# Performance work log

Measured on AMD Instinct MI355X. Metric: run time of the kernel, lower is better.

## Reference

```python
import jax, jax.numpy as jnp
from jax import lax
import numpy as np

B = 32768
H = 7
W = 7
EMB = 64
NUM_ACTIONS = 7
HIDDEN = 128
CNN_OUT = 64 * 3 * 3  # 576, from 7x7 input through the conv/pool stack


def setup_inputs() -> dict:
    key = jax.random.key(0)
    ks = jax.random.split(key, 20)
    frame = jax.random.randint(ks[0], (2, B, H, W, 3), 0, 11, dtype=jnp.int32)
    carried_col = jax.random.randint(ks[1], (2, B, 1), 0, 6, dtype=jnp.int32)
    carried_obj = jax.random.randint(ks[2], (2, B, 1), 0, 11, dtype=jnp.int32)

    def w(k, shape):
        return (jax.random.normal(k, shape, jnp.float32) * 0.05)

    return {
        "frame": frame,
        "carried_col": carried_col,
        "carried_obj": carried_obj,
        "conv1_w": w(ks[3], (16, 3, 2, 2)),  "conv1_b": jnp.zeros((16,), jnp.float32),
        "conv2_w": w(ks[4], (32, 16, 2, 2)), "conv2_b": jnp.zeros((32,), jnp.float32),
        "conv3_w": w(ks[5], (64, 32, 2, 2)), "conv3_b": jnp.zeros((64,), jnp.float32),
        "proj_w": w(ks[6], (EMB, CNN_OUT + 2)), "proj_b": jnp.zeros((EMB,), jnp.float32),
        "h1_w": w(ks[7], (HIDDEN, EMB * 2 + 4)), "h1_b": jnp.zeros((HIDDEN,), jnp.float32),
        "ln_g": jnp.ones((HIDDEN,), jnp.float32), "ln_b": jnp.zeros((HIDDEN,), jnp.float32),
        "h2_w": w(ks[8], (HIDDEN, HIDDEN)), "h2_b": jnp.zeros((HIDDEN,), jnp.float32),
        "h3_w": w(ks[9], (NUM_ACTIONS, HIDDEN)), "h3_b": jnp.zeros((NUM_ACTIONS,), jnp.float32),
    }


def _conv(x, wgt, b):
    # Conv2d(kernel=2, padding=1), NCHW
    y = lax.conv_general_dilated(x, wgt, (1, 1), [(1, 1), (1, 1)],
                                 dimension_numbers=("NCHW", "OIHW", "NCHW"))
    return y + b[None, :, None, None]


def _maxpool2(x):
    # MaxPool2d(2): window 2, stride 2, floor (VALID)
    return lax.reduce_window(x, -jnp.inf, lax.max, (1, 1, 2, 2), (1, 1, 2, 2), "VALID")


def _encode(fr, cc, co, p):
    x = fr.transpose(0, 3, 1, 2).astype(jnp.float32)  # [B,3,H,W]
    x = _maxpool2(jax.nn.relu(_conv(x, p["conv1_w"], p["conv1_b"])))  # [B,16,4,4]
    x = _maxpool2(jax.nn.relu(_conv(x, p["conv2_w"], p["conv2_b"])))  # [B,32,2,2]
    x = jax.nn.relu(_conv(x, p["conv3_w"], p["conv3_b"]))             # [B,64,3,3]
    feats = x.reshape(x.shape[0], -1)                                  # [B,576]
    carried = jnp.concatenate([cc, co], axis=-1).astype(jnp.float32)   # [B,2]
    comb = jnp.concatenate([feats, carried], axis=1)                   # [B,578]
    return jax.nn.relu(comb @ p["proj_w"].T + p["proj_b"])            # [B,64]


def _dir_pos(fr):
    # vectorized first-match of frame[...,0]==10 in row-major order
    b = fr.shape[0]
    mask = (fr[..., 0] == 10).reshape(b, -1)             # [B, H*W]
    has = jnp.any(mask, axis=-1)                         # [B]
    idx = jnp.argmax(mask, axis=-1)                      # first True (row-major)
    y = idx // W
    x = idx % W
    ch2 = fr[..., 2].reshape(b, -1)
    d_raw = jnp.take_along_axis(ch2, idx[:, None], axis=1)[:, 0] % 4
    d = jnp.where(has, d_raw, 0)                         # [B] int
    pos = jnp.stack([y.astype(jnp.float32) / (H - 1),
                     x.astype(jnp.float32) / (W - 1)], axis=-1)
    pos = jnp.where(has[:, None], pos, jnp.float32(0.5))  # [B,2]
    return d, pos


def _forward(frame, carried_col, carried_obj, p):
    curr_f, next_f = frame[0], frame[1]
    curr_emb = _encode(curr_f, carried_col[0], carried_obj[0], p)
    next_emb = _encode(next_f, carried_col[1], carried_obj[1], p)
    cd, cpos = _dir_pos(curr_f)
    nd, npos = _dir_pos(next_f)
    delta = ((nd - cd + 4) % 4).astype(jnp.float32)
    angle = delta * (2.0 * 3.14159 / 4.0)  # matches source constant
    dir_delta = jnp.stack([jnp.sin(angle), jnp.cos(angle)], axis=-1)  # [B,2]
    pos_delta = npos - cpos                                           # [B,2]
    comb = jnp.concatenate([curr_emb, next_emb, dir_delta, pos_delta], axis=-1)  # [B,132]
    h = comb @ p["h1_w"].T + p["h1_b"]
    mu = h.mean(-1, keepdims=True)
    var = ((h - mu) ** 2).mean(-1, keepdims=True)
    h = (h - mu) * lax.rsqrt(var + 1e-5) * p["ln_g"] + p["ln_b"]
    h = jax.nn.relu(h)  # dropout = identity in eval
    h = jax.nn.relu(h @ p["h2_w"].T + p["h2_b"])
    return h @ p["h3_w"].T + p["h3_b"]  # [B, num_actions]


def reference(frame, carried_col, carried_obj,
              conv1_w, conv1_b, conv2_w, conv2_b, conv3_w, conv3_b,
              proj_w, proj_b, h1_w, h1_b, ln_g, ln_b,
              h2_w, h2_b, h3_w, h3_b):
    p = dict(conv1_w=conv1_w, conv1_b=conv1_b, conv2_w=conv2_w, conv2_b=conv2_b,
             conv3_w=conv3_w, conv3_b=conv3_b, proj_w=proj_w, proj_b=proj_b,
             h1_w=h1_w, h1_b=h1_b, ln_g=ln_g, ln_b=ln_b,
             h2_w=h2_w, h2_b=h2_b, h3_w=h3_w, h3_b=h3_b)
    return _forward(frame, carried_col, carried_obj, p)
```

## Files before the change

### kernel.cpp

```cpp
#include <hip/hip_runtime.h>
#include <hip/hip_bf16.h>

#define BATCH 32768
#define NELEM 65536

typedef unsigned short u16;
typedef unsigned int u32;
typedef __attribute__((ext_vector_type(8))) short bf16x8;
typedef __attribute__((ext_vector_type(4))) float f32x4;

__device__ __forceinline__ float bf2f(u16 u) {
    union { u32 u; float f; } c; c.u = ((u32)u) << 16; return c.f;
}
__device__ __forceinline__ u16 f2bf(float f) {
    union { float f; u32 u; } c; c.f = f;
    u32 x = c.u;
    u32 r = (x + 0x7fffu + ((x >> 16) & 1u)) >> 16;
    return (u16)r;
}

__global__ __launch_bounds__(256) void k0_prep(const float* __restrict__ pw,
        const float* __restrict__ w2, const float* __restrict__ w3,
        const float* __restrict__ h2w, const float* __restrict__ h1w,
        const float* __restrict__ w1,
        u16* __restrict__ pwT, u16* __restrict__ w2r, u16* __restrict__ w3r,
        u16* __restrict__ h2hi, u16* __restrict__ h2lo,
        u16* __restrict__ h1hi, u16* __restrict__ h1lo,
        u16* __restrict__ w1hi, u16* __restrict__ w1lo) {
    int idx = blockIdx.x * 256 + threadIdx.x;
    if (idx < 38912) {
        int j = idx / 608, kk = idx - j * 608;
        float v = 0.f;
        if (kk < 576) {
            int p = kk >> 6, oc = kk & 63;
            v = pw[j * 578 + oc * 9 + p];
        } else if (kk < 578) {
            v = pw[j * 578 + kk];
        }
        pwT[idx] = f2bf(v);
    } else if (idx < 40960) {
        int i = idx - 38912;
        int oc = i >> 6, rem = i & 63, tap = rem >> 4, ic = rem & 15;
        w2r[i] = f2bf(w2[oc * 64 + ic * 4 + tap]);
    } else if (idx < 49152) {
        int i = idx - 40960;
        int oc = i >> 7, rem = i & 127, tap = rem >> 5, ic = rem & 31;
        w3r[i] = f2bf(w3[oc * 128 + ic * 4 + tap]);
    } else if (idx < 65536) {
        int i = idx - 49152;
        float v = h2w[i];
        u16 hi = f2bf(v);
        h2hi[i] = hi;
        h2lo[i] = f2bf(v - bf2f(hi));
    } else if (idx < 86016) {
        int i = idx - 65536;
        int j = i / 160, k = i - j * 160;
        float v = (k < 132) ? h1w[j * 132 + k] : 0.f;
        u16 hi = f2bf(v);
        h1hi[i] = hi;
        h1lo[i] = f2bf(v - bf2f(hi));
    } else if (idx < 86528) {
        int i = idx - 86016;
        int oc = i >> 5, k = i & 31;
        int ky = k >> 4, kx = (k >> 3) & 1, c = k & 7;
        float v = (c < 3) ? w1[oc * 12 + c * 4 + ky * 2 + kx] : 0.f;
        u16 hi = f2bf(v);
        w1hi[i] = hi;
        w1lo[i] = f2bf(v - bf2f(hi));
    }
}

__device__ __forceinline__ void split8(const float* __restrict__ x,
                                       bf16x8& hi, bf16x8& lo) {
    #pragma unroll
    for (int j = 0; j < 8; ++j) {
        u16 h = f2bf(x[j]);
        hi[j] = (short)h;
        lo[j] = (short)f2bf(x[j] - bf2f(h));
    }
}

__global__ __launch_bounds__(256) void kall(const int* __restrict__ frame,
        const u16* __restrict__ w1hi, const u16* __restrict__ w1lo,
        const float* __restrict__ b1,
        const u16* __restrict__ w2r, const float* __restrict__ b2,
        const u16* __restrict__ w3r, const float* __restrict__ b3,
        const int* __restrict__ ccol, const int* __restrict__ cobj,
        const u16* __restrict__ pwT, const float* __restrict__ pb,
        const u16* __restrict__ h1hi, const u16* __restrict__ h1lo,
        const float* __restrict__ h1b,
        const float* __restrict__ lng, const float* __restrict__ lnb,
        const u16* __restrict__ h2hi, const u16* __restrict__ h2lo,
        const float* __restrict__ h2b,
        const float* __restrict__ h3w, const float* __restrict__ h3b,
        float* __restrict__ out) {
    __shared__ u16 lds[24576];
    __shared__ float4 fdirL[32];
    u16* p2L   = lds;
    u16* p1L   = lds + 4096;
    u16* frL   = lds + 12288;
    u16* featL = lds + 4096;
    float* combL = (float*)lds;
    float* hL    = (float*)(lds + 4096);
    int t = threadIdx.x;
    int l = t & 63;
    int wv = t >> 6;
    int col = l & 15;
    int kg = l >> 4;
    int b0 = blockIdx.x * 16;

    #pragma unroll
    for (int i = 0; i < 6; ++i) {
        int o = i * 256 + t;
        if (o < 1312) *(uint4*)(frL + o * 8) = make_uint4(0u, 0u, 0u, 0u);
    }

    {
        bf16x8 c1hi = *(const bf16x8*)(w1hi + col * 32 + kg * 8);
        bf16x8 c1lo = *(const bf16x8*)(w1lo + col * 32 + kg * 8);
        float c1b = b1[col];
        int ky1 = kg >> 1, kx1 = kg & 1;
        bool wr1 = (kg < 2);
        for (int h = 0; h < 2; ++h) {
            __syncthreads();
            const int* fbase = frame + ((size_t)b0 + (size_t)h * BATCH) * 147;
            #pragma unroll
            for (int i = 0; i < 10; ++i) {
                int idx = i * 256 + t;
                if (idx < 2352) {
                    int le = idx / 147, r = idx - le * 147;
                    int cell = r / 3, c = r - cell * 3;
                    int y = cell / 7, x = cell - y * 7;
                    frL[le * 656 + (y + 1) * 72 + (x + 1) * 8 + c] = f2bf((float)fbase[idx]);
                }
            }
            __syncthreads();
            #pragma unroll
            for (int q = 0; q < 4; ++q) {
                int le = wv * 4 + q;
                const u16* eb = frL + le * 656;
                u16* op = p1L + (h * 16 + le) * 256;
                #pragma unroll
                for (int mt = 0; mt < 4; ++mt) {
                    int posA = mt * 16 + col;
                    int oy = posA >> 3, ox = posA & 7;
                    bf16x8 a = *(const bf16x8*)(eb + (oy + ky1) * 72 + (ox + kx1) * 8);
                    f32x4 acc = {0.f, 0.f, 0.f, 0.f};
                    acc = __builtin_amdgcn_mfma_f32_16x16x32_bf16(a, c1hi, acc, 0, 0, 0);
                    acc = __builtin_amdgcn_mfma_f32_16x16x32_bf16(a, c1lo, acc, 0, 0, 0);
                    float x0 = fmaxf(acc[0] + c1b, 0.f);
                    float x1 = fmaxf(acc[1] + c1b, 0.f);
                    float x2 = fmaxf(acc[2] + c1b, 0.f);
                    float x3 = fmaxf(acc[3] + c1b, 0.f);
                    float y0 = fmaxf(x0, x1);
                    float y1 = fmaxf(x2, x3);
                    float m0 = fmaxf(y0, __shfl_xor(y0, 32, 64));
                    float m1 = fmaxf(y1, __shfl_xor(y1, 32, 64));
                    if (wr1) {
                        op[(mt * 4 + kg * 2 + 0) * 16 + col] = f2bf(m0);
                        op[(mt * 4 + kg * 2 + 1) * 16 + col] = f2bf(m1);
                    }
                }
            }
            {
                int le = wv * 4 + kg;
                const u16* eb = frL + le * 656;
                int best = 49;
                #pragma unroll
                for (int q2 = 0; q2 < 4; ++q2) {
                    int cell = col + q2 * 16;
                    if (cell < 49) {
                        int y = cell / 7, x = cell - y * 7;
                        u16 v = eb[(y + 1) * 72 + (x + 1) * 8];
                        if (v == (u16)0x4120 && cell < best) best = cell;
                    }
                }
                best = min(best, __shfl_xor(best, 1, 64));
                best = min(best, __shfl_xor(best, 2, 64));
                best = min(best, __shfl_xor(best, 4, 64));
                best = min(best, __shfl_xor(best, 8, 64));
                if (col == 0) {
                    float dd = 0.f, py = 0.5f, px = 0.5f;
                    if (best < 49) {
                        int y = best / 7, x = best - y * 7;
                        u16 c2 = eb[(y + 1) * 72 + (x + 1) * 8 + 2];
                        dd = (float)(((int)bf2f(c2)) & 3);
                        py = (float)y / 6.0f;
                        px = (float)x / 6.0f;
                    }
                    fdirL[h * 16 + le] = make_float4(dd, py, px, 0.f);
                }
            }
        }
    }
    __syncthreads();

    {
        bf16x8 bfrag[2][2];
        #pragma unroll
        for (int s = 0; s < 2; ++s)
            #pragma unroll
            for (int nt = 0; nt < 2; ++nt)
                bfrag[s][nt] = *(const bf16x8*)(w2r + (nt * 16 + col) * 64 + s * 32 + kg * 8);
        float bias2[2] = { b2[col], b2[16 + col] };
        int oy = col >> 2, ox = col & 3;
        int aoff[2]; bool aok[2];
        #pragma unroll
        for (int s = 0; s < 2; ++s) {
            int tap = 2 * s + (kg >> 1);
            int ky = tap >> 1, kx = tap & 1;
            int iy = oy - 1 + ky, ix = ox - 1 + kx;
            aok[s] = (iy >= 0 && ix >= 0);
            aoff[s] = (iy * 4 + ix) * 16 + (kg & 1) * 8;
        }
        #pragma unroll
        for (int q = 0; q < 8; ++q) {
            int e = wv * 8 + q;
            const u16* pbase = p1L + e * 256;
            bf16x8 a0 = {0,0,0,0,0,0,0,0}, a1 = {0,0,0,0,0,0,0,0};
            if (aok[0]) a0 = *(const bf16x8*)(pbase + aoff[0]);
            if (aok[1]) a1 = *(const bf16x8*)(pbase + aoff[1]);
            f32x4 acc0 = {0.f,0.f,0.f,0.f}, acc1 = {0.f,0.f,0.f,0.f};
            acc0 = __builtin_amdgcn_mfma_f32_16x16x32_bf16(a0, bfrag[0][0], acc0, 0, 0, 0);
            acc1 = __builtin_amdgcn_mfma_f32_16x16x32_bf16(a0, bfrag[0][1], acc1, 0, 0, 0);
            acc0 = __builtin_amdgcn_mfma_f32_16x16x32_bf16(a1, bfrag[1][0], acc0, 0, 0, 0);
            acc1 = __builtin_amdgcn_mfma_f32_16x16x32_bf16(a1, bfrag[1][1], acc1, 0, 0, 0);
            #pragma unroll
            for (int nt = 0; nt < 2; ++nt) {
                f32x4 acc = nt ? acc1 : acc0;
                float b = bias2[nt];
                float m0 = fmaxf(fmaxf(acc[0] + b, 0.f), fmaxf(acc[1] + b, 0.f));
                float m1 = fmaxf(fmaxf(acc[2] + b, 0.f), fmaxf(acc[3] + b, 0.f));
                float p0 = fmaxf(m0, __shfl_xor(m0, 16, 64));
                float p1 = fmaxf(m1, __shfl_xor(m1, 16, 64));
                if ((kg & 1) == 0) {
                    int qq = (kg >> 1) * 2;
                    u16* op = p2L + e * 128 + nt * 16 + col;
                    op[qq * 32]       = f2bf(p0);
                    op[(qq + 1) * 32] = f2bf(p1);
                }
            }
        }
    }
    __syncthreads();

    int colhi = col >> 3, collo = col & 7;
    {
        bf16x8 bfrag[4][4];
        #pragma unroll
        for (int s = 0; s < 4; ++s)
            #pragma unroll
            for (int nt = 0; nt < 4; ++nt)
                bfrag[s][nt] = *(const bf16x8*)(w3r + (nt * 16 + col) * 128 + s * 32 + kg * 8);
        float bias[4];
        #pragma unroll
        for (int nt = 0; nt < 4; ++nt) bias[nt] = b3[nt * 16 + col];

        auto do_tile = [&](int i) {
            int m0 = i * 16;
            int m = m0 + col;
            u32 elem = (u32)(((unsigned long long)(u32)m * 954437177ull) >> 33);
            int p = m - (int)elem * 9;
            int oy = (p * 86) >> 8;
            int ox = p - 3 * oy;
            const u16* pbase = p2L + elem * 128 + kg * 8;
            f32x4 acc[4];
            #pragma unroll
            for (int nt = 0; nt < 4; ++nt) {
                acc[nt][0] = 0.f; acc[nt][1] = 0.f; acc[nt][2] = 0.f; acc[nt][3] = 0.f;
            }
            #pragma unroll
            for (int s = 0; s < 4; ++s) {
                int ky = s >> 1, kx = s & 1;
                int iy = oy - 1 + ky, ix = ox - 1 + kx;
                bf16x8 a = {0,0,0,0,0,0,0,0};
                if (iy >= 0 && iy <= 1 && ix >= 0 && ix <= 1)
                    a = *(const bf16x8*)(pbase + (iy * 2 + ix) * 32);
                #pragma unroll
                for (int nt = 0; nt < 4; ++nt)
                    acc[nt] = __builtin_amdgcn_mfma_f32_16x16x32_bf16(a, bfrag[s][nt], acc[nt], 0, 0, 0);
            }
            #pragma unroll
            for (int r = 0; r < 4; ++r) {
                int mr = m0 + kg * 4 + r;
                u32 er = (u32)(((unsigned long long)(u32)mr * 954437177ull) >> 33);
                int pr = mr - (int)er * 9;
                int e7 = (int)(er & 7u);
                u16* fb = featL + er * 640 + collo;
                #pragma unroll
                for (int nt = 0; nt < 4; ++nt) {
                    int blk = (pr * 8 + nt * 2 + colhi) ^ e7;
                    fb[blk * 8] = f2bf(fmaxf(acc[nt][r] + bias[nt], 0.f));
                }
            }
        };
        #pragma unroll
        for (int u = 0; u < 4; ++u) do_tile(wv + u * 4);
        if (wv < 2) do_tile(16 + wv);
    }
    if (t < 32) {
        int g = b0 + (t >> 4) * BATCH + (t & 15);
        union { u16 s[8]; uint4 q; } b;
        b.s[0] = f2bf((float)ccol[g]);
        b.s[1] = f2bf((float)cobj[g]);
        #pragma unroll
        for (int i = 2; i < 8; ++i) b.s[i] = 0;
        *(uint4*)(featL + t * 640 + (72 ^ (t & 7)) * 8) = b.q;
    }
    __syncthreads();

    {
        int rh = wv & 1, nh = wv >> 1;
        const u16* arowb = featL + (rh * 16 + col) * 640;
        int rx = col & 7;
        const u16* brow = pwT + (nh * 32 + col) * 608 + kg * 8;
        f32x4 acc0 = {0.f,0.f,0.f,0.f}, acc1 = {0.f,0.f,0.f,0.f};
        #pragma unroll
        for (int k0 = 0; k0 < 608; k0 += 32) {
            bf16x8 a;
            if (k0 + kg * 8 < 584) {
                int L = (k0 >> 3) + kg;
                a = *(const bf16x8*)(arowb + (L ^ rx) * 8);
            } else {
                #pragma unroll
                for (int j = 0; j < 8; ++j) a[j] = 0;
            }
            bf16x8 b0f = *(const bf16x8*)(brow + k0);
            bf16x8 b1f = *(const bf16x8*)(brow + 16 * 608 + k0);
            acc0 = __builtin_amdgcn_mfma_f32_16x16x32_bf16(a, b0f, acc0, 0, 0, 0);
            acc1 = __builtin_amdgcn_mfma_f32_16x16x32_bf16(a, b1f, acc1, 0, 0, 0);
        }
        __syncthreads();
        #pragma unroll
        for (int nt = 0; nt < 2; ++nt) {
            int n = nh * 32 + nt * 16 + col;
            float pbv = pb[n];
            f32x4 acc = nt ? acc1 : acc0;
            #pragma unroll
            for (int r = 0; r < 4; ++r) {
                combL[(kg * 4 + r) * 128 + rh * 64 + n] = fmaxf(acc[r] + pbv, 0.f);
            }
        }
    }
    __syncthreads();

    {
        const float* arow = combL + col * 128 + kg * 8;
        f32x4 acc[2];
        acc[0][0]=0.f; acc[0][1]=0.f; acc[0][2]=0.f; acc[0][3]=0.f;
        acc[1][0]=0.f; acc[1][1]=0.f; acc[1][2]=0.f; acc[1][3]=0.f;
        #pragma unroll
        for (int s = 0; s < 5; ++s) {
            float x[8];
            if (s < 4) {
                #pragma unroll
                for (int j = 0; j < 8; ++j) x[j] = arow[s * 32 + j];
            } else {
                #pragma unroll
                for (int j = 0; j < 8; ++j) x[j] = 0.f;
                if (kg == 0) {
                    float4 f0 = fdirL[col];
                    float4 f1 = fdirL[16 + col];
                    int delta = (((int)f1.x) - ((int)f0.x) + 4) & 3;
                    const float ANG = (float)(2.0 * 3.14159 / 4.0);
                    float angle = (float)delta * ANG;
                    x[0] = sinf(angle);
                    x[1] = cosf(angle);
                    x[2] = f1.y - f0.y;
                    x[3] = f1.z - f0.z;
                }
            }
            bf16x8 ahi, alo;
            split8(x, ahi, alo);
            #pragma unroll
            for (int nt = 0; nt < 2; ++nt) {
                int n0 = (wv * 2 + nt) * 16 + col;
                bf16x8 bhiF = *(const bf16x8*)(h1hi + n0 * 160 + s * 32 + kg * 8);
                bf16x8 bloF = *(const bf16x8*)(h1lo + n0 * 160 + s * 32 + kg * 8);
                acc[nt] = __builtin_amdgcn_mfma_f32_16x16x32_bf16(ahi, bhiF, acc[nt], 0, 0, 0);
                acc[nt] = __builtin_amdgcn_mfma_f32_16x16x32_bf16(alo, bhiF, acc[nt], 0, 0, 0);
                acc[nt] = __builtin_amdgcn_mfma_f32_16x16x32_bf16(ahi, bloF, acc[nt], 0, 0, 0);
            }
        }
        #pragma unroll
        for (int nt = 0; nt < 2; ++nt) {
            int n = (wv * 2 + nt) * 16 + col;
            float bv = h1b[n];
            #pragma unroll
            for (int r = 0; r < 4; ++r)
                hL[(kg * 4 + r) * 132 + n] = acc[nt][r] + bv;
        }
    }
    __syncthreads();

    #pragma unroll
    for (int rr = 0; rr < 4; ++rr) {
        float* rp = hL + (wv * 4 + rr) * 132 + l * 2;
        float2 v = *(const float2*)rp;
        float s = v.x + v.y;
        s += __shfl_xor(s, 1, 64);
        s += __shfl_xor(s, 2, 64);
        s += __shfl_xor(s, 4, 64);
        s += __shfl_xor(s, 8, 64);
        s += __shfl_xor(s, 16, 64);
        s += __shfl_xor(s, 32, 64);
        float mu = s * (1.0f / 128.0f);
        float d0 = v.x - mu, d1 = v.y - mu;
        float vs = d0 * d0 + d1 * d1;
        vs += __shfl_xor(vs, 1, 64);
        vs += __shfl_xor(vs, 2, 64);
        vs += __shfl_xor(vs, 4, 64);
        vs += __shfl_xor(vs, 8, 64);
        vs += __shfl_xor(vs, 16, 64);
        vs += __shfl_xor(vs, 32, 64);
        float rs = rsqrtf(vs * (1.0f / 128.0f) + 1e-5f);
        float2 o;
        o.x = fmaxf(d0 * rs * lng[l * 2]     + lnb[l * 2],     0.f);
        o.y = fmaxf(d1 * rs * lng[l * 2 + 1] + lnb[l * 2 + 1], 0.f);
        *(float2*)rp = o;
    }
    __syncthreads();

    {
        const float* arow = hL + col * 132 + kg * 8;
        f32x4 acc[2];
        acc[0][0]=0.f; acc[0][1]=0.f; acc[0][2]=0.f; acc[0][3]=0.f;
        acc[1][0]=0.f; acc[1][1]=0.f; acc[1][2]=0.f; acc[1][3]=0.f;
        #pragma unroll
        for (int s = 0; s < 4; ++s) {
            float x[8];
            #pragma unroll
            for (int j = 0; j < 8; ++j) x[j] = arow[s * 32 + j];
            bf16x8 ahi, alo;
            split8(x, ahi, alo);
            #pragma unroll
            for (int nt = 0; nt < 2; ++nt) {
                int n0 = (wv * 2 + nt) * 16 + col;
                bf16x8 bhiF = *(const bf16x8*)(h2hi + n0 * 128 + s * 32 + kg * 8);
                bf16x8 bloF = *(const bf16x8*)(h2lo + n0 * 128 + s * 32 + kg * 8);
                acc[nt] = __builtin_amdgcn_mfma_f32_16x16x32_bf16(ahi, bhiF, acc[nt], 0, 0, 0);
                acc[nt] = __builtin_amdgcn_mfma_f32_16x16x32_bf16(alo, bhiF, acc[nt], 0, 0, 0);
                acc[nt] = __builtin_amdgcn_mfma_f32_16x16x32_bf16(ahi, bloF, acc[nt], 0, 0, 0);
            }
        }
        __syncthreads();
        #pragma unroll
        for (int nt = 0; nt < 2; ++nt) {
            int n = (wv * 2 + nt) * 16 + col;
            float bv = h2b[n];
            #pragma unroll
            for (int r = 0; r < 4; ++r)
                hL[(kg * 4 + r) * 132 + n] = fmaxf(acc[nt][r] + bv, 0.f);
        }
    }
    __syncthreads();

    if (t < 112) {
        int row = t / 7, j = t - row * 7;
        const float* rp = hL + row * 132;
        float a0 = h3b[j];
        const float* wr0 = h3w + j * 128;
        #pragma unroll 4
        for (int c = 0; c < 32; ++c) {
            float4 v = *(const float4*)(rp + c * 4);
            a0 += v.x * wr0[c * 4 + 0];
            a0 += v.y * wr0[c * 4 + 1];
            a0 += v.z * wr0[c * 4 + 2];
            a0 += v.w * wr0[c * 4 + 3];
        }
        out[(size_t)(b0 + row) * 7 + j] = a0;
    }
}

extern "C" void kernel_launch(void* const* d_in, const int* in_sizes, int n_in,
                              void* d_out, int out_size, void* d_ws, size_t ws_size,
                              hipStream_t stream) {
    const int*   frame = (const int*)d_in[0];
    const int*   ccol  = (const int*)d_in[1];
    const int*   cobj  = (const int*)d_in[2];
    const float* w1    = (const float*)d_in[3];
    const float* b1    = (const float*)d_in[4];
    const float* w2    = (const float*)d_in[5];
    const float* b2    = (const float*)d_in[6];
    const float* w3    = (const float*)d_in[7];
    const float* b3    = (const float*)d_in[8];
    const float* pw    = (const float*)d_in[9];
    const float* pb    = (const float*)d_in[10];
    const float* h1w   = (const float*)d_in[11];
    const float* h1b   = (const float*)d_in[12];
    const float* lng   = (const float*)d_in[13];
    const float* lnb   = (const float*)d_in[14];
    const float* h2w   = (const float*)d_in[15];
    const float* h2b   = (const float*)d_in[16];
    const float* h3w   = (const float*)d_in[17];
    const float* h3b   = (const float*)d_in[18];
    float* out = (float*)d_out;

    char* ws = (char*)d_ws;
    u16*   pwT      = (u16*)(ws + 0);
    u16*   w2r      = (u16*)(ws + 131072);
    u16*   w3r      = (u16*)(ws + 139264);
    u16*   h2hi     = (u16*)(ws + 163840);
    u16*   h2lo     = (u16*)(ws + 196608);
    u16*   h1hi     = (u16*)(ws + 229376);
    u16*   h1lo     = (u16*)(ws + 270336);
    u16*   w1hi     = (u16*)(ws + 311296);
    u16*   w1lo     = (u16*)(ws + 312320);

    k0_prep<<<340, 256, 0, stream>>>(pw, w2, w3, h2w, h1w, w1,
                                     pwT, w2r, w3r, h2hi, h2lo, h1hi, h1lo,
                                     w1hi, w1lo);
    kall<<<2048, 256, 0, stream>>>(frame, w1hi, w1lo, b1, w2r, b2,
                                   w3r, b3, ccol, cobj, pwT, pb,
                                   h1hi, h1lo, h1b, lng, lnb,
                                   h2hi, h2lo, h2b, h3w, h3b, out);
}
```

Baseline: 219.3 us.

## Shrink LDS footprint by staging frames in quarters and conv3/proj per half

```diff
diff --git a/kernel.cpp b/kernel.cpp
--- a/kernel.cpp
+++ b/kernel.cpp
@@ -94,14 +94,14 @@
         const float* __restrict__ h2b,
         const float* __restrict__ h3w, const float* __restrict__ h3b,
         float* __restrict__ out) {
-    __shared__ u16 lds[24576];
+    __shared__ u16 lds[19008];
     __shared__ float4 fdirL[32];
-    u16* p2L   = lds;
-    u16* p1L   = lds + 4096;
-    u16* frL   = lds + 12288;
-    u16* featL = lds + 4096;
-    float* combL = (float*)lds;
-    float* hL    = (float*)(lds + 4096);
+    u16* p2L     = lds;
+    float* combL = (float*)(lds + 4096);
+    u16* p1L     = lds + 8192;
+    u16* frL     = lds + 16384;
+    u16* featL   = lds + 8192;
+    float* hL    = (float*)(lds + 8192);
     int t = threadIdx.x;
     int l = t & 63;
     int wv = t >> 6;
@@ -110,9 +110,9 @@
     int b0 = blockIdx.x * 16;
 
     #pragma unroll
-    for (int i = 0; i < 6; ++i) {
+    for (int i = 0; i < 2; ++i) {
         int o = i * 256 + t;
-        if (o < 1312) *(uint4*)(frL + o * 8) = make_uint4(0u, 0u, 0u, 0u);
+        if (o < 328) *(uint4*)(frL + o * 8) = make_uint4(0u, 0u, 0u, 0u);
     }
 
     {
@@ -121,13 +121,14 @@
         float c1b = b1[col];
         int ky1 = kg >> 1, kx1 = kg & 1;
         bool wr1 = (kg < 2);
-        for (int h = 0; h < 2; ++h) {
+        for (int p = 0; p < 8; ++p) {
+            int half = p >> 2, quad = p & 3;
             __syncthreads();
-            const int* fbase = frame + ((size_t)b0 + (size_t)h * BATCH) * 147;
-            #pragma unroll
-            for (int i = 0; i < 10; ++i) {
+            const int* fbase = frame + ((size_t)b0 + (size_t)half * BATCH + quad * 4) * 147;
+            #pragma unroll
+            for (int i = 0; i < 3; ++i) {
                 int idx = i * 256 + t;
-                if (idx < 2352) {
+                if (idx < 588) {
                     int le = idx / 147, r = idx - le * 147;
                     int cell = r / 3, c = r - cell * 3;
                     int y = cell / 7, x = cell - y * 7;
@@ -135,51 +136,42 @@
                 }
             }
             __syncthreads();
-            #pragma unroll
-            for (int q = 0; q < 4; ++q) {
-                int le = wv * 4 + q;
-                const u16* eb = frL + le * 656;
-                u16* op = p1L + (h * 16 + le) * 256;
-                #pragma unroll
-                for (int mt = 0; mt < 4; ++mt) {
-                    int posA = mt * 16 + col;
-                    int oy = posA >> 3, ox = posA & 7;
-                    bf16x8 a = *(const bf16x8*)(eb + (oy + ky1) * 72 + (ox + kx1) * 8);
-                    f32x4 acc = {0.f, 0.f, 0.f, 0.f};
-                    acc = __builtin_amdgcn_mfma_f32_16x16x32_bf16(a, c1hi, acc, 0, 0, 0);
-                    acc = __builtin_amdgcn_mfma_f32_16x16x32_bf16(a, c1lo, acc, 0, 0, 0);
-                    float x0 = fmaxf(acc[0] + c1b, 0.f);
-                    float x1 = fmaxf(acc[1] + c1b, 0.f);
-                    float x2 = fmaxf(acc[2] + c1b, 0.f);
-                    float x3 = fmaxf(acc[3] + c1b, 0.f);
-                    float y0 = fmaxf(x0, x1);
-                    float y1 = fmaxf(x2, x3);
-                    float m0 = fmaxf(y0, __shfl_xor(y0, 32, 64));
-                    float m1 = fmaxf(y1, __shfl_xor(y1, 32, 64));
-                    if (wr1) {
-                        op[(mt * 4 + kg * 2 + 0) * 16 + col] = f2bf(m0);
-                        op[(mt * 4 + kg * 2 + 1) * 16 + col] = f2bf(m1);
-                    }
+            const u16* eb = frL + wv * 656;
+            u16* op = p1L + (half * 16 + quad * 4 + wv) * 256;
+            #pragma unroll
+            for (int mt = 0; mt < 4; ++mt) {
+                int posA = mt * 16 + col;
+                int oy = posA >> 3, ox = posA & 7;
+                bf16x8 a = *(const bf16x8*)(eb + (oy + ky1) * 72 + (ox + kx1) * 8);
+                f32x4 acc = {0.f, 0.f, 0.f, 0.f};
+                acc = __builtin_amdgcn_mfma_f32_16x16x32_bf16(a, c1hi, acc, 0, 0, 0);
+                acc = __builtin_amdgcn_mfma_f32_16x16x32_bf16(a, c1lo, acc, 0, 0, 0);
+                float x0 = fmaxf(acc[0] + c1b, 0.f);
+                float x1 = fmaxf(acc[1] + c1b, 0.f);
+                float x2 = fmaxf(acc[2] + c1b, 0.f);
+                float x3 = fmaxf(acc[3] + c1b, 0.f);
+                float y0 = fmaxf(x0, x1);
+                float y1 = fmaxf(x2, x3);
+                float m0 = fmaxf(y0, __shfl_xor(y0, 32, 64));
+                float m1 = fmaxf(y1, __shfl_xor(y1, 32, 64));
+                if (wr1) {
+                    op[(mt * 4 + kg * 2 + 0) * 16 + col] = f2bf(m0);
+                    op[(mt * 4 + kg * 2 + 1) * 16 + col] = f2bf(m1);
                 }
             }
             {
-                int le = wv * 4 + kg;
-                const u16* eb = frL + le * 656;
                 int best = 49;
-                #pragma unroll
-                for (int q2 = 0; q2 < 4; ++q2) {
-                    int cell = col + q2 * 16;
-                    if (cell < 49) {
-                        int y = cell / 7, x = cell - y * 7;
-                        u16 v = eb[(y + 1) * 72 + (x + 1) * 8];
-                        if (v == (u16)0x4120 && cell < best) best = cell;
-                    }
+                if (l < 49) {
+                    int y = l / 7, x = l - y * 7;
+                    if (eb[(y + 1) * 72 + (x + 1) * 8] == (u16)0x4120) best = l;
                 }
                 best = min(best, __shfl_xor(best, 1, 64));
                 best = min(best, __shfl_xor(best, 2, 64));
                 best = min(best, __shfl_xor(best, 4, 64));
                 best = min(best, __shfl_xor(best, 8, 64));
-                if (col == 0) {
+                best = min(best, __shfl_xor(best, 16, 64));
+                best = min(best, __shfl_xor(best, 32, 64));
+                if (l == 0) {
                     float dd = 0.f, py = 0.5f, px = 0.5f;
                     if (best < 49) {
                         int y = best / 7, x = best - y * 7;
@@ -188,7 +180,7 @@
                         py = (float)y / 6.0f;
                         px = (float)x / 6.0f;
                     }
-                    fdirL[h * 16 + le] = make_float4(dd, py, px, 0.f);
+                    fdirL[half * 16 + quad * 4 + wv] = make_float4(dd, py, px, 0.f);
                 }
             }
         }
@@ -242,103 +234,97 @@
             }
         }
     }
-    __syncthreads();
 
     int colhi = col >> 3, collo = col & 7;
-    {
-        bf16x8 bfrag[4][4];
-        #pragma unroll
-        for (int s = 0; s < 4; ++s)
-            #pragma unroll
-            for (int nt = 0; nt < 4; ++nt)
-                bfrag[s][nt] = *(const bf16x8*)(w3r + (nt * 16 + col) * 128 + s * 32 + kg * 8);
-        float bias[4];
-        #pragma unroll
-        for (int nt = 0; nt < 4; ++nt) bias[nt] = b3[nt * 16 + col];
-
-        auto do_tile = [&](int i) {
-            int m0 = i * 16;
-            int m = m0 + col;
-            u32 elem = (u32)(((unsigned long long)(u32)m * 954437177ull) >> 33);
-            int p = m - (int)elem * 9;
-            int oy = (p * 86) >> 8;
-            int ox = p - 3 * oy;
-            const u16* pbase = p2L + elem * 128 + kg * 8;
-            f32x4 acc[4];
-            #pragma unroll
-            for (int nt = 0; nt < 4; ++nt) {
-                acc[nt][0] = 0.f; acc[nt][1] = 0.f; acc[nt][2] = 0.f; acc[nt][3] = 0.f;
-            }
-            #pragma unroll
-            for (int s = 0; s < 4; ++s) {
-                int ky = s >> 1, kx = s & 1;
-                int iy = oy - 1 + ky, ix = ox - 1 + kx;
-                bf16x8 a = {0,0,0,0,0,0,0,0};
-                if (iy >= 0 && iy <= 1 && ix >= 0 && ix <= 1)
-                    a = *(const bf16x8*)(pbase + (iy * 2 + ix) * 32);
+    for (int half = 0; half < 2; ++half) {
+        __syncthreads();
+        {
+            bf16x8 bfrag[4][4];
+            #pragma unroll
+            for (int s = 0; s < 4; ++s)
                 #pragma unroll
                 for (int nt = 0; nt < 4; ++nt)
-                    acc[nt] = __builtin_amdgcn_mfma_f32_16x16x32_bf16(a, bfrag[s][nt], acc[nt], 0, 0, 0);
-            }
-            #pragma unroll
-            for (int r = 0; r < 4; ++r) {
-                int mr = m0 + kg * 4 + r;
-                u32 er = (u32)(((unsigned long long)(u32)mr * 954437177ull) >> 33);
-                int pr = mr - (int)er * 9;
-                int e7 = (int)(er & 7u);
-                u16* fb = featL + er * 640 + collo;
+                    bfrag[s][nt] = *(const bf16x8*)(w3r + (nt * 16 + col) * 128 + s * 32 + kg * 8);
+            float bias[4];
+            #pragma unroll
+            for (int nt = 0; nt < 4; ++nt) bias[nt] = b3[nt * 16 + col];
+
+            auto do_tile = [&](int i) {
+                int m0 = i * 16;
+                int m = m0 + col;
+                u32 elem = (u32)(((unsigned long long)(u32)m * 954437177ull) >> 33);
+                int p = m - (int)elem * 9;
+                int oy = (p * 86) >> 8;
+                int ox = p - 3 * oy;
+                const u16* pbase = p2L + (half * 16 + (int)elem) * 128 + kg * 8;
+                f32x4 acc[4];
                 #pragma unroll
                 for (int nt = 0; nt < 4; ++nt) {
-                    int blk = (pr * 8 + nt * 2 + colhi) ^ e7;
-                    fb[blk * 8] = f2bf(fmaxf(acc[nt][r] + bias[nt], 0.f));
-                }
-            }
-        };
-        #pragma unroll
-        for (int u = 0; u < 4; ++u) do_tile(wv + u * 4);
-        if (wv < 2) do_tile(16 + wv);
-    }
-    if (t < 32) {
-        int g = b0 + (t >> 4) * BATCH + (t & 15);
-        union { u16 s[8]; uint4 q; } b;
-        b.s[0] = f2bf((float)ccol[g]);
-        b.s[1] = f2bf((float)cobj[g]);
-        #pragma unroll
-        for (int i = 2; i < 8; ++i) b.s[i] = 0;
-        *(uint4*)(featL + t * 640 + (72 ^ (t & 7)) * 8) = b.q;
-    }
-    __syncthreads();
-
-    {
-        int rh = wv & 1, nh = wv >> 1;
-        const u16* arowb = featL + (rh * 16 + col) * 640;
-        int rx = col & 7;
-        const u16* brow = pwT + (nh * 32 + col) * 608 + kg * 8;
-        f32x4 acc0 = {0.f,0.f,0.f,0.f}, acc1 = {0.f,0.f,0.f,0.f};
-        #pragma unroll
-        for (int k0 = 0; k0 < 608; k0 += 32) {
-            bf16x8 a;
-            if (k0 + kg * 8 < 584) {
-                int L = (k0 >> 3) + kg;
-                a = *(const bf16x8*)(arowb + (L ^ rx) * 8);
-            } else {
+                    acc[nt][0] = 0.f; acc[nt][1] = 0.f; acc[nt][2] = 0.f; acc[nt][3] = 0.f;
+                }
                 #pragma unroll
-                for (int j = 0; j < 8; ++j) a[j] = 0;
-            }
-            bf16x8 b0f = *(const bf16x8*)(brow + k0);
-            bf16x8 b1f = *(const bf16x8*)(brow + 16 * 608 + k0);
-            acc0 = __builtin_amdgcn_mfma_f32_16x16x32_bf16(a, b0f, acc0, 0, 0, 0);
-            acc1 = __builtin_amdgcn_mfma_f32_16x16x32_bf16(a, b1f, acc1, 0, 0, 0);
+                for (int s = 0; s < 4; ++s) {
+                    int ky = s >> 1, kx = s & 1;
+                    int iy = oy - 1 + ky, ix = ox - 1 + kx;
+                    bf16x8 a = {0,0,0,0,0,0,0,0};
+                    if (iy >= 0 && iy <= 1 && ix >= 0 && ix <= 1)
+                        a = *(const bf16x8*)(pbase + (iy * 2 + ix) * 32);
+                    #pragma unroll
+                    for (int nt = 0; nt < 4; ++nt)
+                        acc[nt] = __builtin_amdgcn_mfma_f32_16x16x32_bf16(a, bfrag[s][nt], acc[nt], 0, 0, 0);
+                }
+                #pragma unroll
+                for (int r = 0; r < 4; ++r) {
+                    int mr = m0 + kg * 4 + r;
+                    u32 er = (u32)(((unsigned long long)(u32)mr * 954437177ull) >> 33);
+                    int pr = mr - (int)er * 9;
+                    int e7 = (int)(er & 7u);
+                    u16* fb = featL + er * 640 + collo;
+                    #pragma unroll
+                    for (int nt = 0; nt < 4; ++nt) {
+                        int blk = (pr * 8 + nt * 2 + colhi) ^ e7;
+                        fb[blk * 8] = f2bf(fmaxf(acc[nt][r] + bias[nt], 0.f));
+                    }
+                }
+            };
+            do_tile(wv);
+            do_tile(wv + 4);
+            if (wv == 0) do_tile(8);
+        }
+        if (t < 16) {
+            int g = b0 + half * BATCH + t;
+            union { u16 s[8]; uint4 q; } b;
+            b.s[0] = f2bf((float)ccol[g]);
+            b.s[1] = f2bf((float)cobj[g]);
+            #pragma unroll
+            for (int i = 2; i < 8; ++i) b.s[i] = 0;
+            *(uint4*)(featL + t * 640 + (72 ^ (t & 7)) * 8) = b.q;
         }
         __syncthreads();
-        #pragma unroll
-        for (int nt = 0; nt < 2; ++nt) {
-            int n = nh * 32 + nt * 16 + col;
+
+        {
+            const u16* arowb = featL + col * 640;
+            int rx = col & 7;
+            const u16* brow = pwT + (wv * 16 + col) * 608 + kg * 8;
+            f32x4 acc = {0.f, 0.f, 0.f, 0.f};
+            #pragma unroll
+            for (int k0 = 0; k0 < 608; k0 += 32) {
+                bf16x8 a;
+                if (k0 + kg * 8 < 584) {
+                    int L = (k0 >> 3) + kg;
+                    a = *(const bf16x8*)(arowb + (L ^ rx) * 8);
+                } else {
+                    #pragma unroll
+                    for (int j = 0; j < 8; ++j) a[j] = 0;
+                }
+                bf16x8 bf = *(const bf16x8*)(brow + k0);
+                acc = __builtin_amdgcn_mfma_f32_16x16x32_bf16(a, bf, acc, 0, 0, 0);
+            }
+            int n = wv * 16 + col;
             float pbv = pb[n];
-            f32x4 acc = nt ? acc1 : acc0;
             #pragma unroll
             for (int r = 0; r < 4; ++r) {
-                combL[(kg * 4 + r) * 128 + rh * 64 + n] = fmaxf(acc[r] + pbv, 0.f);
+                combL[(kg * 4 + r) * 128 + half * 64 + n] = fmaxf(acc[r] + pbv, 0.f);
             }
         }
     }
@@ -382,6 +368,7 @@
                 acc[nt] = __builtin_amdgcn_mfma_f32_16x16x32_bf16(ahi, bloF, acc[nt], 0, 0, 0);
             }
         }
+        __syncthreads();
         #pragma unroll
         for (int nt = 0; nt < 2; ++nt) {
             int n = (wv * 2 + nt) * 16 + col;
```

Result: slower. 270.1 us (+23.2%).
